# Optimization experiments

Measured on AMD Instinct MI355X. Metric: run time of the kernel, lower is better.

## Reference

```python
import jax, jax.numpy as jnp
import numpy as np

K = 2  # KNNGraph(2): each point connects to its 2 nearest neighbors (self included)


def setup_inputs() -> dict:
    key = jax.random.key(0)
    N, D = 16384, 64
    X = jax.random.normal(key, (N, D), dtype=jnp.float32)
    return {"X": X}


def reference(X) -> jnp.ndarray:
    # Pairwise squared Euclidean distances (ordering identical to cdist for top-k).
    sq = jnp.sum(X * X, axis=-1)                      # [N]
    dist2 = sq[:, None] + sq[None, :] - 2.0 * (X @ X.T)  # [N, N]
    # k smallest distances -> k largest of the negated distances
    _, idx = jax.lax.top_k(-dist2, K)                 # [N, K] neighbor indices (self included)
    N = X.shape[0]
    rows = jnp.broadcast_to(jnp.arange(N)[:, None], (N, K))
    # Dense adjacency with 1.0 at (i, nn_j(i)) entries.
    adj = jnp.zeros((N, N), dtype=X.dtype).at[rows, idx].set(1.0)
    return adj
```

## Files before the change

kernel.cpp:

```cpp
#include <hip/hip_runtime.h>
#include <math.h>


#define NPTS 16384
#define DIM 64
#define BI 64
#define BJ 128
#define NTHR 256
#define JSPLIT 4
#define JRANGE (NPTS / JSPLIT)
#define NJT (JRANGE / BJ)
#define BPITCH 136

typedef __attribute__((ext_vector_type(8))) short s16x8;
typedef __attribute__((ext_vector_type(4))) float f32x4;

#define LDS_BARRIER() asm volatile("s_waitcnt lgkmcnt(0)\n\ts_barrier" ::: "memory")

__device__ __forceinline__ ushort bf16_rn(float x) {
  unsigned u = __float_as_uint(x);
  u += 0x7fffu + ((u >> 16) & 1u);
  return (ushort)(u >> 16);
}
__device__ __forceinline__ float bf16_f(ushort h) {
  return __uint_as_float((unsigned)h << 16);
}

__global__ void sq_kernel(const float* __restrict__ X, float* __restrict__ sqout) {
  int i = blockIdx.x * NTHR + threadIdx.x;
  const float4* x4 = (const float4*)(X + (size_t)i * DIM);
  float s = 0.f;
#pragma unroll
  for (int k = 0; k < DIM / 4; ++k) {
    float4 v = x4[k];
    s = fmaf(v.x, v.x, s); s = fmaf(v.y, v.y, s);
    s = fmaf(v.z, v.z, s); s = fmaf(v.w, v.w, s);
  }
  sqout[i] = s;
}

__global__ __launch_bounds__(NTHR, 4) void knn_kernel(
    const float* __restrict__ X, const float* __restrict__ sqn,
    float* __restrict__ out, float* __restrict__ cand_val, int* __restrict__ cand_idx) {
  __shared__ __align__(16) short Bs[BJ * BPITCH];
  __shared__ float sqt[BJ];

  const int tid = threadIdx.x;
  const int lane = tid & 63;
  const int wid = tid >> 6;
  const int li = lane & 15;
  const int g = lane >> 4;
  const int ib = blockIdx.x >> 2;
  const int jh = blockIdx.x & 3;
  const int i0 = ib * BI;
  const int j0base = jh * JRANGE;
  const int i_glob = i0 + wid * 16 + li;
  const size_t z0 = (size_t)jh * JRANGE;

  s16x8 ihiA, iloA, ihiB, iloB;
  {
    const float* xi = X + (size_t)i_glob * DIM;
#pragma unroll
    for (int e = 0; e < 8; ++e) {
      float a = xi[8 * g + e];
      ushort h = bf16_rn(a);
      ihiA[e] = (short)h;
      iloA[e] = (short)bf16_rn(a - bf16_f(h));
      float b = xi[32 + 8 * g + e];
      ushort h2 = bf16_rn(b);
      ihiB[e] = (short)h2;
      iloB[e] = (short)bf16_rn(b - bf16_f(h2));
    }
  }

  float bv = INFINITY;
  int bix = 0x7fffffff;

#pragma unroll 1
  for (int jt = 0; jt < NJT; ++jt) {
    const int j0 = j0base + jt * BJ;
    LDS_BARRIER();
    {
      const float4* src = (const float4*)(X + (size_t)j0 * DIM);
#pragma unroll
      for (int p = 0; p < (BJ * DIM / 4) / NTHR; ++p) {
        int f4 = tid + NTHR * p;
        int r = f4 >> 4, c = f4 & 15;
        float4 v = src[f4];
        ushort hx = bf16_rn(v.x), hy = bf16_rn(v.y), hz = bf16_rn(v.z), hw = bf16_rn(v.w);
        ushort lx = bf16_rn(v.x - bf16_f(hx)), ly = bf16_rn(v.y - bf16_f(hy)),
               lz = bf16_rn(v.z - bf16_f(hz)), lw = bf16_rn(v.w - bf16_f(hw));
        uint2 hq = make_uint2((unsigned)hx | ((unsigned)hy << 16),
                              (unsigned)hz | ((unsigned)hw << 16));
        uint2 lq = make_uint2((unsigned)lx | ((unsigned)ly << 16),
                              (unsigned)lz | ((unsigned)lw << 16));
        *(uint2*)(&Bs[r * BPITCH + c * 4]) = hq;
        *(uint2*)(&Bs[r * BPITCH + 64 + c * 4]) = lq;
      }
      if (tid < BJ) sqt[tid] = sqn[j0 + tid];
    }
    LDS_BARRIER();

    {
#pragma unroll
      for (int p = 0; p < 8; ++p) {
        int f4 = tid + NTHR * p;
        int r = f4 >> 10;
        int c = f4 & 1023;
        *(float4*)(out + (size_t)(i0 + 2 * jt + r) * NPTS + z0 + (size_t)c * 4) =
            make_float4(0.f, 0.f, 0.f, 0.f);
      }
    }

#pragma unroll
    for (int s = 0; s < BJ / 16; ++s) {
      const short* jrow = &Bs[(16 * s + li) * BPITCH];
      s16x8 jhiA = *(const s16x8*)(jrow + 8 * g);
      s16x8 jhiB = *(const s16x8*)(jrow + 32 + 8 * g);
      s16x8 jloA = *(const s16x8*)(jrow + 64 + 8 * g);
      s16x8 jloB = *(const s16x8*)(jrow + 96 + 8 * g);
      f32x4 sqv = *(const f32x4*)(&sqt[16 * s + 4 * g]);
      f32x4 acc = {0.f, 0.f, 0.f, 0.f};
      acc = __builtin_amdgcn_mfma_f32_16x16x32_bf16(jhiA, ihiA, acc, 0, 0, 0);
      acc = __builtin_amdgcn_mfma_f32_16x16x32_bf16(jhiB, ihiB, acc, 0, 0, 0);
      acc = __builtin_amdgcn_mfma_f32_16x16x32_bf16(jloA, ihiA, acc, 0, 0, 0);
      acc = __builtin_amdgcn_mfma_f32_16x16x32_bf16(jloB, ihiB, acc, 0, 0, 0);
      acc = __builtin_amdgcn_mfma_f32_16x16x32_bf16(jhiA, iloA, acc, 0, 0, 0);
      acc = __builtin_amdgcn_mfma_f32_16x16x32_bf16(jhiB, iloB, acc, 0, 0, 0);
#pragma unroll
      for (int r = 0; r < 4; ++r) {
        float d2 = fmaf(-2.f, acc[r], sqv[r]);
        int j = j0 + 16 * s + 4 * g + r;
        if (j != i_glob && d2 < bv) { bv = d2; bix = j; }
      }
    }
  }

  {
    float ov = __shfl_xor(bv, 16, 64);
    int oi = __shfl_xor(bix, 16, 64);
    if (ov < bv || (ov == bv && oi < bix)) { bv = ov; bix = oi; }
    ov = __shfl_xor(bv, 32, 64);
    oi = __shfl_xor(bix, 32, 64);
    if (ov < bv || (ov == bv && oi < bix)) { bv = ov; bix = oi; }
  }
  if (g == 0) {
    cand_val[(size_t)i_glob * JSPLIT + jh] = bv;
    cand_idx[(size_t)i_glob * JSPLIT + jh] = bix;
  }
}

__global__ void merge_kernel(const float* __restrict__ cand_val,
                             const int* __restrict__ cand_idx,
                             float* __restrict__ out) {
  int i = blockIdx.x * NTHR + threadIdx.x;
  float bv = INFINITY;
  int bi = 0x7fffffff;
#pragma unroll
  for (int s = 0; s < JSPLIT; ++s) {
    float v = cand_val[(size_t)i * JSPLIT + s];
    int ix = cand_idx[(size_t)i * JSPLIT + s];
    if (v < bv || (v == bv && ix < bi)) { bv = v; bi = ix; }
  }
  out[(size_t)i * NPTS + i] = 1.0f;
  out[(size_t)i * NPTS + bi] = 1.0f;
}

extern "C" void kernel_launch(void* const* d_in, const int* in_sizes, int n_in,
                              void* d_out, int out_size, void* d_ws, size_t ws_size,
                              hipStream_t stream) {
  const float* X = (const float*)d_in[0];
  float* out = (float*)d_out;

  float* sq = (float*)d_ws;
  float* cand_val = sq + NPTS;
  int* cand_idx = (int*)(cand_val + (size_t)NPTS * JSPLIT);

  sq_kernel<<<NPTS / NTHR, NTHR, 0, stream>>>(X, sq);
  knn_kernel<<<(NPTS / BI) * JSPLIT, NTHR, 0, stream>>>(X, sq, out, cand_val, cand_idx);
  merge_kernel<<<NPTS / NTHR, NTHR, 0, stream>>>(cand_val, cand_idx, out);
}
```

Baseline: 1.186 ms.

## Pre-split X into bf16 hi/lo once and use swizzled LDS tiles

Adds a split_kernel that converts X into a packed bf16 hi/lo array once, so the knn kernel copies pre-split rows into LDS instead of redoing the float-to-bf16 split for every tile in every block. The LDS layout moves from a padded pitch to an XOR swizzle to avoid bank conflicts, and the output zero-fill stores are spread across the MFMA loop so they can overlap with compute. The cost is an extra kernel launch and a workspace buffer, and the tile loads now read 16-bit data, which doubles the bytes per element compared with a single bf16 copy but still matches the original fp32 read size.

Result: faster. 1.083 ms (-8.7%).

```diff
diff --git a/kernel.cpp b/kernel.cpp
--- a/kernel.cpp
+++ b/kernel.cpp
@@ -10,7 +10,7 @@
 #define JSPLIT 4
 #define JRANGE (NPTS / JSPLIT)
 #define NJT (JRANGE / BJ)
-#define BPITCH 136
+#define RPITCH 128
 
 typedef __attribute__((ext_vector_type(8))) short s16x8;
 typedef __attribute__((ext_vector_type(4))) float f32x4;
@@ -24,6 +24,25 @@
 }
 __device__ __forceinline__ float bf16_f(ushort h) {
   return __uint_as_float((unsigned)h << 16);
+}
+
+__global__ void split_kernel(const float* __restrict__ X, short* __restrict__ Xs) {
+  const int tid = threadIdx.x;
+  const int r0 = blockIdx.x * 64;
+#pragma unroll
+  for (int p = 0; p < 4; ++p) {
+    int f4 = tid + NTHR * p;
+    int r = f4 >> 4, c = f4 & 15;
+    float4 v = ((const float4*)(X + (size_t)(r0 + r) * DIM))[c];
+    ushort hx = bf16_rn(v.x), hy = bf16_rn(v.y), hz = bf16_rn(v.z), hw = bf16_rn(v.w);
+    ushort lx = bf16_rn(v.x - bf16_f(hx)), ly = bf16_rn(v.y - bf16_f(hy)),
+           lz = bf16_rn(v.z - bf16_f(hz)), lw = bf16_rn(v.w - bf16_f(hw));
+    short* dst = Xs + (size_t)(r0 + r) * RPITCH;
+    *(uint2*)(dst + 4 * c) = make_uint2((unsigned)hx | ((unsigned)hy << 16),
+                                        (unsigned)hz | ((unsigned)hw << 16));
+    *(uint2*)(dst + 64 + 4 * c) = make_uint2((unsigned)lx | ((unsigned)ly << 16),
+                                             (unsigned)lz | ((unsigned)lw << 16));
+  }
 }
 
 __global__ void sq_kernel(const float* __restrict__ X, float* __restrict__ sqout) {
@@ -40,9 +59,9 @@
 }
 
 __global__ __launch_bounds__(NTHR, 4) void knn_kernel(
-    const float* __restrict__ X, const float* __restrict__ sqn,
+    const short* __restrict__ Xs, const float* __restrict__ sqn,
     float* __restrict__ out, float* __restrict__ cand_val, int* __restrict__ cand_idx) {
-  __shared__ __align__(16) short Bs[BJ * BPITCH];
+  __shared__ __align__(16) short Bs[BJ * RPITCH];
   __shared__ float sqt[BJ];
 
   const int tid = threadIdx.x;
@@ -57,20 +76,14 @@
   const int i_glob = i0 + wid * 16 + li;
   const size_t z0 = (size_t)jh * JRANGE;
 
-  s16x8 ihiA, iloA, ihiB, iloB;
+  const short* xi = Xs + (size_t)i_glob * RPITCH;
+  s16x8 ihiA, ihiB, iloA, iloB;
   {
-    const float* xi = X + (size_t)i_glob * DIM;
-#pragma unroll
-    for (int e = 0; e < 8; ++e) {
-      float a = xi[8 * g + e];
-      ushort h = bf16_rn(a);
-      ihiA[e] = (short)h;
-      iloA[e] = (short)bf16_rn(a - bf16_f(h));
-      float b = xi[32 + 8 * g + e];
-      ushort h2 = bf16_rn(b);
-      ihiB[e] = (short)h2;
-      iloB[e] = (short)bf16_rn(b - bf16_f(h2));
-    }
+    uint4 t;
+    t = *(const uint4*)(xi + 8 * g);        ihiA = *(s16x8*)&t;
+    t = *(const uint4*)(xi + 32 + 8 * g);   ihiB = *(s16x8*)&t;
+    t = *(const uint4*)(xi + 64 + 8 * g);   iloA = *(s16x8*)&t;
+    t = *(const uint4*)(xi + 96 + 8 * g);   iloB = *(s16x8*)&t;
   }
 
   float bv = INFINITY;
@@ -81,44 +94,32 @@
     const int j0 = j0base + jt * BJ;
     LDS_BARRIER();
     {
-      const float4* src = (const float4*)(X + (size_t)j0 * DIM);
+      const uint4* src = (const uint4*)(Xs + (size_t)j0 * RPITCH);
 #pragma unroll
-      for (int p = 0; p < (BJ * DIM / 4) / NTHR; ++p) {
-        int f4 = tid + NTHR * p;
-        int r = f4 >> 4, c = f4 & 15;
-        float4 v = src[f4];
-        ushort hx = bf16_rn(v.x), hy = bf16_rn(v.y), hz = bf16_rn(v.z), hw = bf16_rn(v.w);
-        ushort lx = bf16_rn(v.x - bf16_f(hx)), ly = bf16_rn(v.y - bf16_f(hy)),
-               lz = bf16_rn(v.z - bf16_f(hz)), lw = bf16_rn(v.w - bf16_f(hw));
-        uint2 hq = make_uint2((unsigned)hx | ((unsigned)hy << 16),
-                              (unsigned)hz | ((unsigned)hw << 16));
-        uint2 lq = make_uint2((unsigned)lx | ((unsigned)ly << 16),
-                              (unsigned)lz | ((unsigned)lw << 16));
-        *(uint2*)(&Bs[r * BPITCH + c * 4]) = hq;
-        *(uint2*)(&Bs[r * BPITCH + 64 + c * 4]) = lq;
+      for (int p = 0; p < 8; ++p) {
+        int ck = tid + NTHR * p;
+        int r = ck >> 4, c = ck & 15;
+        uint4 v = src[ck];
+        *(uint4*)(&Bs[r * RPITCH + ((c ^ (r & 7)) << 3)]) = v;
       }
       if (tid < BJ) sqt[tid] = sqn[j0 + tid];
     }
     LDS_BARRIER();
 
-    {
-#pragma unroll
-      for (int p = 0; p < 8; ++p) {
-        int f4 = tid + NTHR * p;
-        int r = f4 >> 10;
-        int c = f4 & 1023;
-        *(float4*)(out + (size_t)(i0 + 2 * jt + r) * NPTS + z0 + (size_t)c * 4) =
+#pragma unroll 2
+    for (int s = 0; s < BJ / 16; ++s) {
+      {
+        int f4 = tid + NTHR * s;
+        int zr = f4 >> 10, zc = f4 & 1023;
+        *(float4*)(out + (size_t)(i0 + 2 * jt + zr) * NPTS + z0 + (size_t)zc * 4) =
             make_float4(0.f, 0.f, 0.f, 0.f);
       }
-    }
-
-#pragma unroll
-    for (int s = 0; s < BJ / 16; ++s) {
-      const short* jrow = &Bs[(16 * s + li) * BPITCH];
-      s16x8 jhiA = *(const s16x8*)(jrow + 8 * g);
-      s16x8 jhiB = *(const s16x8*)(jrow + 32 + 8 * g);
-      s16x8 jloA = *(const s16x8*)(jrow + 64 + 8 * g);
-      s16x8 jloB = *(const s16x8*)(jrow + 96 + 8 * g);
+      const short* jrow = &Bs[(16 * s + li) * RPITCH];
+      const int sw = (li & 7);
+      s16x8 jhiA = *(const s16x8*)(jrow + (((g) ^ sw) << 3));
+      s16x8 jhiB = *(const s16x8*)(jrow + (((4 + g) ^ sw) << 3));
+      s16x8 jloA = *(const s16x8*)(jrow + (((8 + g) ^ sw) << 3));
+      s16x8 jloB = *(const s16x8*)(jrow + (((12 + g) ^ sw) << 3));
       f32x4 sqv = *(const f32x4*)(&sqt[16 * s + 4 * g]);
       f32x4 acc = {0.f, 0.f, 0.f, 0.f};
       acc = __builtin_amdgcn_mfma_f32_16x16x32_bf16(jhiA, ihiA, acc, 0, 0, 0);
@@ -175,8 +176,10 @@
   float* sq = (float*)d_ws;
   float* cand_val = sq + NPTS;
   int* cand_idx = (int*)(cand_val + (size_t)NPTS * JSPLIT);
+  short* Xs = (short*)(cand_idx + (size_t)NPTS * JSPLIT);
 
+  split_kernel<<<NPTS / 64, NTHR, 0, stream>>>(X, Xs);
   sq_kernel<<<NPTS / NTHR, NTHR, 0, stream>>>(X, sq);
-  knn_kernel<<<(NPTS / BI) * JSPLIT, NTHR, 0, stream>>>(X, sq, out, cand_val, cand_idx);
+  knn_kernel<<<(NPTS / BI) * JSPLIT, NTHR, 0, stream>>>(Xs, sq, out, cand_val, cand_idx);
   merge_kernel<<<NPTS / NTHR, NTHR, 0, stream>>>(cand_val, cand_idx, out);
 }
```
